# Optimization experiments

Measured on AMD Instinct MI355X. Metric: run time of the kernel, lower is better.

The kernel has to match this reference:

```python
import jax, jax.numpy as jnp
import numpy as np

N = 4096        # num_nodes
U = 64          # num_units
D = 64          # input_dim
B = 32          # batch
K = 2           # max_diffusion_step
M = K + 1       # num_matrices (1 support * K + identity)


def _build_support(seed=0):
    # random symmetric nonneg sparse adjacency (~avg degree 16), then scaled Laplacian
    rng = np.random.default_rng(seed)
    density = 16.0 / N
    mask = rng.random((N, N)) < density
    A = rng.random((N, N)).astype(np.float32) * mask
    A = np.maximum(A, A.T)
    np.fill_diagonal(A, 0.0)
    d = A.sum(axis=1)
    d_inv_sqrt = np.where(d > 0, 1.0 / np.sqrt(np.maximum(d, 1e-12)), 0.0)
    L = np.eye(N, dtype=np.float32) - (d_inv_sqrt[:, None] * A) * d_inv_sqrt[None, :]
    # scaled Laplacian with lambda_max ~= 2 (standard ChebNet approximation): L_s = 2/lmax * L - I
    return (L - np.eye(N, dtype=np.float32)).astype(np.float32)


def setup_inputs() -> dict:
    key = jax.random.key(0)
    k1, k2, k3, k4 = jax.random.split(key, 4)
    S = D + U  # concat(inputs, state) feature size = 128
    return {
        "inputs": jax.random.normal(k1, (B, N * D), dtype=jnp.float32),
        "hx": jax.random.normal(k2, (B, N * U), dtype=jnp.float32),
        "support": jnp.asarray(_build_support()),
        "W_ru": jax.random.normal(k3, (S * M, 2 * U), dtype=jnp.float32) * (2.0 / (S * M + 2 * U)) ** 0.5,
        "b_ru": jnp.ones((2 * U,), dtype=jnp.float32),  # bias_start=1.0 for GRU gates
        "W_c": jax.random.normal(k4, (S * M, U), dtype=jnp.float32) * (2.0 / (S * M + U)) ** 0.5,
        "b_c": jnp.zeros((U,), dtype=jnp.float32),
    }


def _gconv(support, x_in, state, W, b):
    # x_in: (B, N, D), state: (B, N, U)
    x0 = jnp.concatenate([x_in, state], axis=2)          # (B, N, S)
    S = x0.shape[2]
    x0 = x0.transpose(1, 2, 0).reshape(N, S * B)         # (N, S*B)
    xs = [x0]
    xk_m1, xk = x0, support @ x0                          # T_1 = L x
    xs.append(xk)
    for _ in range(K - 1):                                # Chebyshev recursion
        xk_p1 = 2.0 * (support @ xk) - xk_m1
        xs.append(xk_p1)
        xk_m1, xk = xk, xk_p1
    x = jnp.stack(xs, axis=0)                             # (M, N, S*B)
    x = x.reshape(M, N, S, B).transpose(3, 1, 2, 0)       # (B, N, S, M)
    x = x.reshape(B * N, S * M)
    return x @ W + b                                      # (B*N, out)


def reference(inputs, hx, support, W_ru, b_ru, W_c, b_c):
    x_in = inputs.reshape(B, N, D)
    h = hx.reshape(B, N, U)
    ru = jax.nn.sigmoid(_gconv(support, x_in, h, W_ru, b_ru)).reshape(B, N, 2 * U)
    r, u = jnp.split(ru, 2, axis=2)                       # reset, update gates
    c = jnp.tanh(_gconv(support, x_in, r * h, W_c, b_c)).reshape(B, N, U)
    new_h = u * h + (1.0 - u) * c
    return new_h.reshape(B, N * U)
```

## Files before the change

### kernel.cpp

```cpp
#include <hip/hip_runtime.h>

#define NN 4096
#define BB 32
#define UU 64
#define MAXNNZ 96

typedef float f32x4 __attribute__((ext_vector_type(4)));
typedef float f32x2 __attribute__((ext_vector_type(2)));
typedef short bf16x8 __attribute__((ext_vector_type(8)));
typedef unsigned short us8 __attribute__((ext_vector_type(8)));
typedef unsigned short us4 __attribute__((ext_vector_type(4)));

__device__ __forceinline__ float bf2f(unsigned short u) {
    return __uint_as_float(((unsigned)u) << 16);
}
__device__ __forceinline__ unsigned short f2bf(float f) {
    unsigned x = __float_as_uint(f);
    x += 0x7fffu + ((x >> 16) & 1u);
    return (unsigned short)(x >> 16);
}


__global__ void build_ell(const float* __restrict__ sup, int* __restrict__ cols,
                          float* __restrict__ vals, int* __restrict__ cnt) {
    int row  = blockIdx.x * 4 + (threadIdx.x >> 6);
    int lane = threadIdx.x & 63;
    const float* rp = sup + (size_t)row * NN;
    int base = 0;
    for (int ch = 0; ch < NN / 64; ++ch) {
        float v = rp[ch * 64 + lane];
        unsigned long long m = __ballot(v != 0.0f);
        int pos = __popcll(m & ((1ull << lane) - 1ull));
        if (v != 0.0f) {
            int idx = base + pos;
            if (idx < MAXNNZ) {
                cols[row * MAXNNZ + idx] = ch * 64 + lane;
                vals[row * MAXNNZ + idx] = v;
            }
        }
        base += __popcll(m);
    }
    int kcp = base < MAXNNZ ? ((base + 7) & ~7) : MAXNNZ;
    for (int idx = (base < MAXNNZ ? base : MAXNNZ) + lane; idx < kcp; idx += 64) {
        cols[row * MAXNNZ + idx] = 0;
        vals[row * MAXNNZ + idx] = 0.0f;
    }
    if (lane == 0) cnt[row] = kcp;
}

__global__ void build_x0(const float* __restrict__ inp, const float* __restrict__ hxp,
                         unsigned short* __restrict__ Xall) {
    size_t tt = (size_t)blockIdx.x * 256 + threadIdx.x;
    size_t e  = tt * 4;
    int half  = e >= (size_t)8388608;
    size_t id = e & 8388607ull;
    const float* src = half ? hxp : inp;
    float4 f = *(const float4*)(src + id);
    int d = (int)(id & 63);
    int n = (int)((id >> 6) & 4095);
    int b = (int)(id >> 18);
    int off = half * 2048 + (d >> 5) * 1024 + (b >> 4) * 512 + ((d >> 3) & 3) * 128 +
              (b & 15) * 8 + (d & 7);
    us4 o;
    o[0] = f2bf(f.x); o[1] = f2bf(f.y); o[2] = f2bf(f.z); o[3] = f2bf(f.w);
    *(us4*)(Xall + (size_t)n * 4096 + off) = o;
}

__global__ void prep_w(const float* __restrict__ Wru, const float* __restrict__ Wc,
                       unsigned short* __restrict__ Wp1, unsigned short* __restrict__ Wp2) {
    int t = blockIdx.x * 256 + threadIdx.x;
    int e  = t & 7;
    int li = (t >> 3) & 63;
    int lr = li & 15, kg = li >> 4;
    if (t < 49152) {
        int q = t >> 9;
        int ct = q / 12, kk = q - ct * 12;
        int u = ct * 16 + lr;
        int k = kk * 32 + kg * 8 + e;
        int s = k & 127, m = k >> 7;
        Wp1[t] = f2bf(Wru[(s * 3 + m) * 128 + u]);
    } else {
        int tt = t - 49152;
        int q = tt >> 9;
        int ct = q / 12, kk = q - ct * 12;
        int u = ct * 16 + lr;
        int k = kk * 32 + kg * 8 + e;
        int s = k & 127, m = k >> 7;
        Wp2[tt] = f2bf(Wc[(s * 3 + m) * 64 + u]);
    }
}

template <bool CHEB, int NCOLS>
__launch_bounds__(256, 6)
__global__ void spmm_kernel(const int* __restrict__ cols, const float* __restrict__ vals,
                            const int* __restrict__ cnt, const unsigned short* __restrict__ X,
                            const unsigned short* __restrict__ Z0,
                            unsigned short* __restrict__ Y) {
    int T = gridDim.x;
    int fid = blockIdx.x;
    int v = (fid & 7) * (T >> 3) + (fid >> 3);
    int chunk = v >> 10;
    int rg = v & 1023;
    int row = __builtin_amdgcn_readfirstlane(rg * 4 + (threadIdx.x >> 6));
    int lane = threadIdx.x & 63;
    int c = chunk * 512 + lane * 8;
    const int* cp = cols + row * MAXNNZ;
    const float* vp = vals + row * MAXNNZ;
    const int kc = cnt[row];
    f32x2 acc0 = {0.f, 0.f}, acc1 = {0.f, 0.f}, acc2 = {0.f, 0.f}, acc3 = {0.f, 0.f};

    us8 zreg;
    if (CHEB) zreg = __builtin_nontemporal_load((const us8*)(Z0 + (size_t)row * NCOLS + c));

#define LD(K) (*(const us8*)(X + (size_t)cp[K] * NCOLS + c))
#define FMA1(BV, SV)                                                         \
    {                                                                        \
        f32x2 w = {SV, SV};                                                  \
        const unsigned* p = (const unsigned*)&BV;                            \
        f32x2 xv;                                                            \
        xv.x = __uint_as_float(p[0] << 16);                                  \
        xv.y = __uint_as_float(p[0] & 0xffff0000u);                          \
        acc0 = __builtin_elementwise_fma(w, xv, acc0);                       \
        xv.x = __uint_as_float(p[1] << 16);                                  \
        xv.y = __uint_as_float(p[1] & 0xffff0000u);                          \
        acc1 = __builtin_elementwise_fma(w, xv, acc1);                       \
        xv.x = __uint_as_float(p[2] << 16);                                  \
        xv.y = __uint_as_float(p[2] & 0xffff0000u);                          \
        acc2 = __builtin_elementwise_fma(w, xv, acc2);                       \
        xv.x = __uint_as_float(p[3] << 16);                                  \
        xv.y = __uint_as_float(p[3] & 0xffff0000u);                          \
        acc3 = __builtin_elementwise_fma(w, xv, acc3);                       \
    }

    if (kc) {
        us8 b0 = LD(0), b1 = LD(1), b2 = LD(2), b3 = LD(3);
        us8 b4 = LD(4), b5 = LD(5), b6 = LD(6), b7 = LD(7);
        float s0 = vp[0], s1 = vp[1], s2 = vp[2], s3 = vp[3];
        float s4 = vp[4], s5 = vp[5], s6 = vp[6], s7 = vp[7];
        int k = 0;
        for (; k + 16 <= kc; k += 8) {
            FMA1(b0, s0); b0 = LD(k + 8);  s0 = vp[k + 8];
            FMA1(b1, s1); b1 = LD(k + 9);  s1 = vp[k + 9];
            FMA1(b2, s2); b2 = LD(k + 10); s2 = vp[k + 10];
            FMA1(b3, s3); b3 = LD(k + 11); s3 = vp[k + 11];
            FMA1(b4, s4); b4 = LD(k + 12); s4 = vp[k + 12];
            FMA1(b5, s5); b5 = LD(k + 13); s5 = vp[k + 13];
            FMA1(b6, s6); b6 = LD(k + 14); s6 = vp[k + 14];
            FMA1(b7, s7); b7 = LD(k + 15); s7 = vp[k + 15];
        }
        FMA1(b0, s0); FMA1(b1, s1); FMA1(b2, s2); FMA1(b3, s3);
        FMA1(b4, s4); FMA1(b5, s5); FMA1(b6, s6); FMA1(b7, s7);
    }
#undef LD
#undef FMA1

    float a[8] = {acc0.x, acc0.y, acc1.x, acc1.y, acc2.x, acc2.y, acc3.x, acc3.y};
    if (CHEB) {
        const unsigned* pz = (const unsigned*)&zreg;
#pragma unroll
        for (int i = 0; i < 4; ++i) {
            a[2 * i]     = 2.f * a[2 * i]     - __uint_as_float(pz[i] << 16);
            a[2 * i + 1] = 2.f * a[2 * i + 1] - __uint_as_float(pz[i] & 0xffff0000u);
        }
    }
    us8 o;
#pragma unroll
    for (int i = 0; i < 8; ++i) o[i] = f2bf(a[i]);
    __builtin_nontemporal_store(o, (us8*)(Y + (size_t)row * NCOLS + c));
}

template <int MODE>
__launch_bounds__(512, 6)
__global__ void gemm_kernel(
    const unsigned short* __restrict__ baseIn, size_t bufIn, int rowIn,
    const unsigned short* __restrict__ baseSt, size_t bufSt, int rowSt,
    const unsigned short* __restrict__ Wp, const float* __restrict__ bias,
    const unsigned short* __restrict__ hpk, unsigned short* __restrict__ ubuf,
    unsigned short* __restrict__ x2st, float* __restrict__ outp) {
    __shared__ __align__(16) unsigned short Wl[24576];
    const int t = threadIdx.x;
    const int w = t >> 6, l = t & 63;
    const int bid = blockIdx.x;
    int h, ng;
    if (MODE == 0) { h = (bid >> 3) & 1; ng = (bid & 7) | ((bid >> 4) << 3); }
    else           { h = 0;             ng = bid; }
    const unsigned short* wsrc = Wp + (MODE == 0 ? h * 24576 : 0);
#pragma unroll
    for (int i = 0; i < 6; ++i) {
        int idx = i * 512 + t;
        *(us8*)(&Wl[idx * 8]) = *(const us8*)(wsrc + idx * 8);
    }
    __syncthreads();

    const int n = ng * 8 + w;
    f32x4 acc[4][2];
#pragma unroll
    for (int ct = 0; ct < 4; ++ct)
#pragma unroll
        for (int g = 0; g < 2; ++g)
#pragma unroll
            for (int r2 = 0; r2 < 4; ++r2) acc[ct][g][r2] = 0.f;

    for (int si = 0; si < 6; ++si) {
        const unsigned short* s = (si & 1)
            ? baseSt + (size_t)(si >> 1) * bufSt + (size_t)n * rowSt
            : baseIn + (size_t)(si >> 1) * bufIn + (size_t)n * rowIn;
        us8 aB[4];
#pragma unroll
        for (int dg = 0; dg < 4; ++dg)
            aB[dg] = *(const us8*)(s + dg * 512 + l * 8);
#pragma unroll
        for (int dwin = 0; dwin < 2; ++dwin) {
            const int kk = si * 2 + dwin;
            bf16x8 wf[4];
#pragma unroll
            for (int ct = 0; ct < 4; ++ct)
                wf[ct] = *(const bf16x8*)(&Wl[ct * 6144 + kk * 512 + l * 8]);
#pragma unroll
            for (int ct = 0; ct < 4; ++ct)
#pragma unroll
                for (int g = 0; g < 2; ++g)
                    acc[ct][g] = __builtin_amdgcn_mfma_f32_16x16x32_bf16(
                        wf[ct], (bf16x8)aB[dwin * 2 + g], acc[ct][g], 0, 0, 0);
        }
    }

    const int kg = l >> 4, lr = l & 15;
#pragma unroll
    for (int ct = 0; ct < 4; ++ct) {
        const int u0 = ct * 16 + kg * 4;
        const int pofs = (ct >> 1) * 1024 + ((ct & 1) * 2 + (kg >> 1)) * 128 +
                         lr * 8 + (kg & 1) * 4;
#pragma unroll
        for (int g = 0; g < 2; ++g) {
            if (MODE == 0) {
                if (h == 0) {
                    us4 hv = *(const us4*)(hpk + (size_t)n * 4096 + g * 512 + pofs);
                    us4 o;
#pragma unroll
                    for (int rr = 0; rr < 4; ++rr) {
                        float vv = acc[ct][g][rr] + bias[u0 + rr];
                        float sg = 1.f / (1.f + __expf(-vv));
                        o[rr] = f2bf(sg * bf2f(hv[rr]));
                    }
                    *(us4*)(x2st + (size_t)n * 2048 + g * 512 + pofs) = o;
                } else {
                    us4 o;
#pragma unroll
                    for (int rr = 0; rr < 4; ++rr) {
                        float vv = acc[ct][g][rr] + bias[64 + u0 + rr];
                        float sg = 1.f / (1.f + __expf(-vv));
                        o[rr] = f2bf(sg);
                    }
                    *(us4*)(ubuf + (size_t)n * 2048 + g * 512 + pofs) = o;
                }
            } else {
                const int b = g * 16 + lr;
                us4 hv = *(const us4*)(hpk + (size_t)n * 4096 + g * 512 + pofs);
                us4 uv = *(const us4*)(ubuf + (size_t)n * 2048 + g * 512 + pofs);
                float4 o;
#pragma unroll
                for (int rr = 0; rr < 4; ++rr) {
                    float vv = acc[ct][g][rr] + bias[u0 + rr];
                    float e2 = __expf(2.f * vv);
                    float cc = 1.f - 2.f / (e2 + 1.f);
                    float uu = bf2f(uv[rr]);
                    ((float*)&o)[rr] = uu * bf2f(hv[rr]) + (1.f - uu) * cc;
                }
                *(float4*)(outp + (size_t)b * (NN * UU) + (size_t)n * UU + u0) = o;
            }
        }
    }
}

extern "C" void kernel_launch(void* const* d_in, const int* in_sizes, int n_in,
                              void* d_out, int out_size, void* d_ws, size_t ws_size,
                              hipStream_t stream) {
    const float* inputs  = (const float*)d_in[0];
    const float* hx      = (const float*)d_in[1];
    const float* support = (const float*)d_in[2];
    const float* W_ru    = (const float*)d_in[3];
    const float* b_ru    = (const float*)d_in[4];
    const float* W_c     = (const float*)d_in[5];
    const float* b_c     = (const float*)d_in[6];
    float* out = (float*)d_out;

    char* ws = (char*)d_ws;
    size_t off = 0;
    auto alloc = [&](size_t bytes) -> char* {
        char* p = ws + off;
        off = (off + bytes + 255) & ~(size_t)255;
        return p;
    };
    const size_t BIG = (size_t)NN * 4096;
    const size_t SML = (size_t)NN * 2048;
    int*            colsI = (int*)  alloc((size_t)NN * MAXNNZ * 4);
    float*          valsF = (float*)alloc((size_t)NN * MAXNNZ * 4);
    int*            cntI  = (int*)  alloc((size_t)NN * 4);
    unsigned short* Wp1   = (unsigned short*)alloc(49152 * 2);
    unsigned short* Wp2   = (unsigned short*)alloc(24576 * 2);
    unsigned short* bufA  = (unsigned short*)alloc(3 * BIG * 2);
    unsigned short* bufB  = (unsigned short*)alloc(3 * SML * 2);
    unsigned short* ubuf  = (unsigned short*)alloc(SML * 2);
    if (off > ws_size) return;

    unsigned short* Xall = bufA;
    unsigned short* Z1   = bufA + BIG;
    unsigned short* Z2   = bufA + 2 * BIG;
    unsigned short* X2st = bufB;
    unsigned short* Z1st = bufB + SML;
    unsigned short* Z2st = bufB + 2 * SML;
    unsigned short* Hpk  = Xall + 2048;

    build_ell<<<1024, 256, 0, stream>>>(support, colsI, valsF, cntI);
    build_x0<<<16384, 256, 0, stream>>>(inputs, hx, Xall);
    prep_w<<<288, 256, 0, stream>>>(W_ru, W_c, Wp1, Wp2);

    spmm_kernel<false, 4096><<<8192, 256, 0, stream>>>(colsI, valsF, cntI, Xall, Xall, Z1);
    spmm_kernel<true, 4096><<<8192, 256, 0, stream>>>(colsI, valsF, cntI, Z1, Xall, Z2);
    gemm_kernel<0><<<1024, 512, 0, stream>>>(Xall, BIG, 4096, Xall + 2048, BIG, 4096,
                                             Wp1, b_ru, Hpk, ubuf, X2st, nullptr);
    spmm_kernel<false, 2048><<<4096, 256, 0, stream>>>(colsI, valsF, cntI, X2st, X2st, Z1st);
    spmm_kernel<true, 2048><<<4096, 256, 0, stream>>>(colsI, valsF, cntI, Z1st, X2st, Z2st);
    gemm_kernel<1><<<512, 512, 0, stream>>>(Xall, BIG, 4096, X2st, SML, 2048,
                                            Wp2, b_c, Hpk, ubuf, nullptr, out);
}
```

Measured before the change: 283.9 us.

## Merge prep kernels into one launch and shrink SpMM padding and prefetch depth

Combines the ELL build, activation packing and weight packing kernels into a single launch, with block-index ranges selecting the task, so launch gaps go away and the three independent jobs can run concurrently. It also pads each ELL row to a multiple of 4 instead of 8 and cuts the SpMM software pipeline from 8 to 4 outstanding gathers, which reduces wasted zero-padding work and register pressure. The shallower prefetch may hide less gather latency.

```diff
diff --git a/kernel.cpp b/kernel.cpp
--- a/kernel.cpp
+++ b/kernel.cpp
@@ -21,72 +21,75 @@
 }
 
 
-__global__ void build_ell(const float* __restrict__ sup, int* __restrict__ cols,
-                          float* __restrict__ vals, int* __restrict__ cnt) {
-    int row  = blockIdx.x * 4 + (threadIdx.x >> 6);
-    int lane = threadIdx.x & 63;
-    const float* rp = sup + (size_t)row * NN;
-    int base = 0;
-    for (int ch = 0; ch < NN / 64; ++ch) {
-        float v = rp[ch * 64 + lane];
-        unsigned long long m = __ballot(v != 0.0f);
-        int pos = __popcll(m & ((1ull << lane) - 1ull));
-        if (v != 0.0f) {
-            int idx = base + pos;
-            if (idx < MAXNNZ) {
-                cols[row * MAXNNZ + idx] = ch * 64 + lane;
-                vals[row * MAXNNZ + idx] = v;
+__global__ void prep_all(const float* __restrict__ sup, const float* __restrict__ inp,
+                         const float* __restrict__ hxp, const float* __restrict__ Wru,
+                         const float* __restrict__ Wc, int* __restrict__ cols,
+                         float* __restrict__ vals, int* __restrict__ cnt,
+                         unsigned short* __restrict__ Xall,
+                         unsigned short* __restrict__ Wp1,
+                         unsigned short* __restrict__ Wp2) {
+    const int bid = blockIdx.x;
+    if (bid < 1024) {
+        int row  = bid * 4 + (threadIdx.x >> 6);
+        int lane = threadIdx.x & 63;
+        const float* rp = sup + (size_t)row * NN;
+        int base = 0;
+        for (int ch = 0; ch < NN / 64; ++ch) {
+            float v = rp[ch * 64 + lane];
+            unsigned long long m = __ballot(v != 0.0f);
+            int pos = __popcll(m & ((1ull << lane) - 1ull));
+            if (v != 0.0f) {
+                int idx = base + pos;
+                if (idx < MAXNNZ) {
+                    cols[row * MAXNNZ + idx] = ch * 64 + lane;
+                    vals[row * MAXNNZ + idx] = v;
+                }
             }
-        }
-        base += __popcll(m);
-    }
-    int kcp = base < MAXNNZ ? ((base + 7) & ~7) : MAXNNZ;
-    for (int idx = (base < MAXNNZ ? base : MAXNNZ) + lane; idx < kcp; idx += 64) {
-        cols[row * MAXNNZ + idx] = 0;
-        vals[row * MAXNNZ + idx] = 0.0f;
-    }
-    if (lane == 0) cnt[row] = kcp;
-}
-
-__global__ void build_x0(const float* __restrict__ inp, const float* __restrict__ hxp,
-                         unsigned short* __restrict__ Xall) {
-    size_t tt = (size_t)blockIdx.x * 256 + threadIdx.x;
-    size_t e  = tt * 4;
-    int half  = e >= (size_t)8388608;
-    size_t id = e & 8388607ull;
-    const float* src = half ? hxp : inp;
-    float4 f = *(const float4*)(src + id);
-    int d = (int)(id & 63);
-    int n = (int)((id >> 6) & 4095);
-    int b = (int)(id >> 18);
-    int off = half * 2048 + (d >> 5) * 1024 + (b >> 4) * 512 + ((d >> 3) & 3) * 128 +
-              (b & 15) * 8 + (d & 7);
-    us4 o;
-    o[0] = f2bf(f.x); o[1] = f2bf(f.y); o[2] = f2bf(f.z); o[3] = f2bf(f.w);
-    *(us4*)(Xall + (size_t)n * 4096 + off) = o;
-}
-
-__global__ void prep_w(const float* __restrict__ Wru, const float* __restrict__ Wc,
-                       unsigned short* __restrict__ Wp1, unsigned short* __restrict__ Wp2) {
-    int t = blockIdx.x * 256 + threadIdx.x;
-    int e  = t & 7;
-    int li = (t >> 3) & 63;
-    int lr = li & 15, kg = li >> 4;
-    if (t < 49152) {
-        int q = t >> 9;
-        int ct = q / 12, kk = q - ct * 12;
-        int u = ct * 16 + lr;
-        int k = kk * 32 + kg * 8 + e;
-        int s = k & 127, m = k >> 7;
-        Wp1[t] = f2bf(Wru[(s * 3 + m) * 128 + u]);
+            base += __popcll(m);
+        }
+        int kb  = base < MAXNNZ ? base : MAXNNZ;
+        int kcp = base < MAXNNZ ? ((base + 3) & ~3) : MAXNNZ;
+        for (int idx = kb + lane; idx < kcp; idx += 64) {
+            cols[row * MAXNNZ + idx] = 0;
+            vals[row * MAXNNZ + idx] = 0.0f;
+        }
+        if (lane == 0) cnt[row] = kcp;
+    } else if (bid < 17408) {
+        size_t tt = (size_t)(bid - 1024) * 256 + threadIdx.x;
+        size_t e  = tt * 4;
+        int half  = e >= (size_t)8388608;
+        size_t id = e & 8388607ull;
+        const float* src = half ? hxp : inp;
+        float4 f = *(const float4*)(src + id);
+        int d = (int)(id & 63);
+        int n = (int)((id >> 6) & 4095);
+        int b = (int)(id >> 18);
+        int off = half * 2048 + (d >> 5) * 1024 + (b >> 4) * 512 +
+                  ((d >> 3) & 3) * 128 + (b & 15) * 8 + (d & 7);
+        us4 o;
+        o[0] = f2bf(f.x); o[1] = f2bf(f.y); o[2] = f2bf(f.z); o[3] = f2bf(f.w);
+        *(us4*)(Xall + (size_t)n * 4096 + off) = o;
     } else {
-        int tt = t - 49152;
-        int q = tt >> 9;
-        int ct = q / 12, kk = q - ct * 12;
-        int u = ct * 16 + lr;
-        int k = kk * 32 + kg * 8 + e;
-        int s = k & 127, m = k >> 7;
-        Wp2[tt] = f2bf(Wc[(s * 3 + m) * 64 + u]);
+        int t = (bid - 17408) * 256 + threadIdx.x;
+        int e  = t & 7;
+        int li = (t >> 3) & 63;
+        int lr = li & 15, kg = li >> 4;
+        if (t < 49152) {
+            int q = t >> 9;
+            int ct = q / 12, kk = q - ct * 12;
+            int u = ct * 16 + lr;
+            int k = kk * 32 + kg * 8 + e;
+            int s = k & 127, m = k >> 7;
+            Wp1[t] = f2bf(Wru[(s * 3 + m) * 128 + u]);
+        } else {
+            int tt2 = t - 49152;
+            int q = tt2 >> 9;
+            int ct = q / 12, kk = q - ct * 12;
+            int u = ct * 16 + lr;
+            int k = kk * 32 + kg * 8 + e;
+            int s = k & 127, m = k >> 7;
+            Wp2[tt2] = f2bf(Wc[(s * 3 + m) * 64 + u]);
+        }
     }
 }
 
@@ -134,22 +137,15 @@
 
     if (kc) {
         us8 b0 = LD(0), b1 = LD(1), b2 = LD(2), b3 = LD(3);
-        us8 b4 = LD(4), b5 = LD(5), b6 = LD(6), b7 = LD(7);
         float s0 = vp[0], s1 = vp[1], s2 = vp[2], s3 = vp[3];
-        float s4 = vp[4], s5 = vp[5], s6 = vp[6], s7 = vp[7];
         int k = 0;
-        for (; k + 16 <= kc; k += 8) {
-            FMA1(b0, s0); b0 = LD(k + 8);  s0 = vp[k + 8];
-            FMA1(b1, s1); b1 = LD(k + 9);  s1 = vp[k + 9];
-            FMA1(b2, s2); b2 = LD(k + 10); s2 = vp[k + 10];
-            FMA1(b3, s3); b3 = LD(k + 11); s3 = vp[k + 11];
-            FMA1(b4, s4); b4 = LD(k + 12); s4 = vp[k + 12];
-            FMA1(b5, s5); b5 = LD(k + 13); s5 = vp[k + 13];
-            FMA1(b6, s6); b6 = LD(k + 14); s6 = vp[k + 14];
-            FMA1(b7, s7); b7 = LD(k + 15); s7 = vp[k + 15];
+        for (; k + 8 <= kc; k += 4) {
+            FMA1(b0, s0); b0 = LD(k + 4); s0 = vp[k + 4];
+            FMA1(b1, s1); b1 = LD(k + 5); s1 = vp[k + 5];
+            FMA1(b2, s2); b2 = LD(k + 6); s2 = vp[k + 6];
+            FMA1(b3, s3); b3 = LD(k + 7); s3 = vp[k + 7];
         }
         FMA1(b0, s0); FMA1(b1, s1); FMA1(b2, s2); FMA1(b3, s3);
-        FMA1(b4, s4); FMA1(b5, s5); FMA1(b6, s6); FMA1(b7, s7);
     }
 #undef LD
 #undef FMA1
@@ -312,9 +308,8 @@
     unsigned short* Z2st = bufB + 2 * SML;
     unsigned short* Hpk  = Xall + 2048;
 
-    build_ell<<<1024, 256, 0, stream>>>(support, colsI, valsF, cntI);
-    build_x0<<<16384, 256, 0, stream>>>(inputs, hx, Xall);
-    prep_w<<<288, 256, 0, stream>>>(W_ru, W_c, Wp1, Wp2);
+    prep_all<<<17696, 256, 0, stream>>>(support, inputs, hx, W_ru, W_c,
+                                        colsI, valsF, cntI, Xall, Wp1, Wp2);
 
     spmm_kernel<false, 4096><<<8192, 256, 0, stream>>>(colsI, valsF, cntI, Xall, Xall, Z1);
     spmm_kernel<true, 4096><<<8192, 256, 0, stream>>>(colsI, valsF, cntI, Z1, Xall, Z2);
```

Result: faster. 273.3 us (-3.7%).
